# Performance work log

Measured on AMD Instinct MI355X. Metric: run time of the kernel, lower is better.

## Reference

```python
import math
import jax, jax.numpy as jnp
import numpy as np

HEADS = 8
DIM = 512
HEAD_SIZE = DIM // HEADS  # 64


def setup_inputs() -> dict:
    key = jax.random.key(0)
    ks = jax.random.split(key, 5)
    b, nh, nw, t, d = 16, 16, 16, 16, DIM
    x = jax.random.normal(ks[0], (b, nh, nw, t, d), dtype=jnp.float32)
    s = 1.0 / math.sqrt(d)
    Wq = jax.random.normal(ks[1], (d, d), dtype=jnp.float32) * s
    Wk = jax.random.normal(ks[2], (d, d), dtype=jnp.float32) * s
    Wv = jax.random.normal(ks[3], (d, d), dtype=jnp.float32) * s
    Wo = jax.random.normal(ks[4], (d, d), dtype=jnp.float32) * s
    z = jnp.zeros((d,), dtype=jnp.float32)
    return {"x": x, "Wq": Wq, "bq": z, "Wk": Wk, "bk": z, "Wv": Wv, "bv": z, "Wo": Wo, "bo": z}


def _split_heads(t):
    # [b, n1, n2, T, D] -> [b, n1, n2, H, T, hs]
    b, n1, n2, T, _ = t.shape
    return t.reshape(b, n1, n2, T, HEADS, HEAD_SIZE).transpose(0, 1, 2, 4, 3, 5)


def reference(x, Wq, bq, Wk, bk, Wv, bv, Wo, bo):
    q = _split_heads(x @ Wq + bq)
    k = _split_heads(x @ Wk + bk)
    v = _split_heads(x @ Wv + bv)
    # windowed attention scores: [b, n1, n2, H, T, T]
    scores = jnp.einsum('bnmhtd,bnmhsd->bnmhts', q, k) / math.sqrt(HEAD_SIZE)
    probs = jax.nn.sigmoid(scores)  # NOTE: elementwise sigmoid, not softmax
    ctx = jnp.einsum('bnmhts,bnmhsd->bnmhtd', probs, v)
    b, n1, n2, H, T, hs = ctx.shape
    ctx = ctx.transpose(0, 1, 2, 4, 3, 5).reshape(b, n1, n2, T, H * hs)
    return ctx @ Wo + bo
```

## Files before the change

### kernel.cpp

```cpp
#include <hip/hip_runtime.h>
#include <hip/hip_bf16.h>

typedef float f32x4 __attribute__((ext_vector_type(4)));
typedef __bf16 bf16x8 __attribute__((ext_vector_type(8)));
typedef unsigned short u16x4 __attribute__((ext_vector_type(4)));
typedef unsigned short u16x8 __attribute__((ext_vector_type(8)));

__device__ __forceinline__ unsigned short f2bf(float f) {
  union { float f; unsigned u; } x; x.f = f;
  unsigned r = x.u + 0x7FFFu + ((x.u >> 16) & 1u);
  return (unsigned short)(r >> 16);
}

__device__ __forceinline__ void gl16(const void* g, void* l) {
  __builtin_amdgcn_global_load_lds(
      (const __attribute__((address_space(1))) unsigned*)g,
      (__attribute__((address_space(3))) unsigned*)l, 16, 0, 0);
}

__global__ __launch_bounds__(256) void prep_wt(const float* __restrict__ Wq,
                                               const float* __restrict__ Wk,
                                               const float* __restrict__ Wv,
                                               const float* __restrict__ Wo,
                                               unsigned short* __restrict__ WT) {
  __shared__ unsigned short ts[64][65];
  const float* W = (blockIdx.z == 0) ? Wq : (blockIdx.z == 1) ? Wk
                   : (blockIdx.z == 2) ? Wv : Wo;
  const int t = threadIdx.x;
  const int kbase = blockIdx.y * 64;
  const int nbase = blockIdx.x * 64;
  for (int i = 0; i < 16; ++i) {
    int idx = i * 256 + t;
    int r = idx >> 6, c = idx & 63;
    ts[r][c] = f2bf(W[(size_t)(kbase + r) * 512 + nbase + c]);
  }
  __syncthreads();
  unsigned short* dst = WT + (size_t)blockIdx.z * 512 * 512;
  for (int i = 0; i < 16; ++i) {
    int idx = i * 256 + t;
    int nn = idx >> 6, kk = idx & 63;
    dst[(size_t)(nbase + nn) * 512 + kbase + kk] = ts[kk][nn];
  }
}

__global__ void prep_bias(const float* __restrict__ bq, const float* __restrict__ bk,
                          const float* __restrict__ bv, float* __restrict__ biasc) {
  int i = blockIdx.x * 256 + threadIdx.x;
  if (i < 512) biasc[i] = bq[i];
  else if (i < 1024) biasc[i] = bk[i - 512];
  else if (i < 1536) biasc[i] = bv[i - 1024];
}

__global__ __launch_bounds__(256) void convert_x(const float* __restrict__ x,
                                                 unsigned short* __restrict__ xb,
                                                 long long n8) {
  long long i = (long long)blockIdx.x * 256 + threadIdx.x;
  const long long stride = (long long)gridDim.x * 256;
  for (; i < n8; i += stride) {
    f32x4 a = *reinterpret_cast<const f32x4*>(&x[i * 8]);
    f32x4 b = *reinterpret_cast<const f32x4*>(&x[i * 8 + 4]);
    u16x8 o;
    o[0] = f2bf(a[0]); o[1] = f2bf(a[1]); o[2] = f2bf(a[2]); o[3] = f2bf(a[3]);
    o[4] = f2bf(b[0]); o[5] = f2bf(b[1]); o[6] = f2bf(b[2]); o[7] = f2bf(b[3]);
    *reinterpret_cast<u16x8*>(&xb[i * 8]) = o;
  }
}

template <typename CT>
__global__ __launch_bounds__(256, 4) void gemm128(
    const unsigned short* __restrict__ A, int lda,
    const unsigned short* __restrict__ BT,
    CT* __restrict__ C, int ldc,
    const float* __restrict__ bias, int NB) {
  __shared__ alignas(16) unsigned short pool[16640];
  const int t = threadIdx.x;
  const int lane = t & 63;
  const int w = t >> 6;
  const int wm = w >> 1, wn = w & 1;

  const int nwg = gridDim.x;
  const int cpx = nwg >> 3;
  const int wg = (blockIdx.x & 7) * cpx + (blockIdx.x >> 3);
  const int n0 = (wg % NB) * 128;
  const int m0 = (wg / NB) * 128;

  const int sgr = lane >> 2;
  const int sgc = ((lane & 3) ^ ((lane >> 3) & 3)) << 3;
  const unsigned short* gA = A + (size_t)(m0 + w * 32 + sgr) * lda + sgc;
  const unsigned short* gB = BT + (size_t)(n0 + w * 32 + sgr) * 512 + sgc;
  const int lw = w * 1024;

#define SA(kt, b)                                                           \
  { const unsigned short* g_ = gA + (kt) * 32;                              \
    gl16(g_, &pool[(b) * 4096 + lw]);                                       \
    gl16(g_ + (size_t)16 * lda, &pool[(b) * 4096 + lw + 512]); }
#define SB(kt, b)                                                           \
  { const unsigned short* g_ = gB + (kt) * 32;                              \
    gl16(g_, &pool[8192 + (b) * 4096 + lw]);                                \
    gl16(g_ + (size_t)16 * 512, &pool[8192 + (b) * 4096 + lw + 512]); }

  const int fr = lane & 15;
  const int fg = lane >> 4;
  const int aslot = (fg ^ ((fr >> 1) & 3)) << 3;

  f32x4 acc[4][4];
#pragma unroll
  for (int i = 0; i < 4; ++i)
#pragma unroll
    for (int j = 0; j < 4; ++j) acc[i][j] = (f32x4){0.f, 0.f, 0.f, 0.f};
  bf16x8 afr[4], bfr[4];

  SA(0, 0) SB(0, 0)
  asm volatile("s_waitcnt vmcnt(0)" ::: "memory");
  __builtin_amdgcn_s_barrier();

#pragma unroll
  for (int kt = 0; kt < 16; ++kt) {
    const int b = kt & 1;
    if (kt < 15) { SA(kt + 1, b ^ 1) SB(kt + 1, b ^ 1) }
#pragma unroll
    for (int mi = 0; mi < 4; ++mi)
      afr[mi] = *reinterpret_cast<const bf16x8*>(
          &pool[b * 4096 + (wm * 64 + mi * 16 + fr) * 32 + aslot]);
#pragma unroll
    for (int ni = 0; ni < 4; ++ni)
      bfr[ni] = *reinterpret_cast<const bf16x8*>(
          &pool[8192 + b * 4096 + (wn * 64 + ni * 16 + fr) * 32 + aslot]);
    asm volatile("s_waitcnt lgkmcnt(0)" ::: "memory");
    __builtin_amdgcn_sched_barrier(0);
    __builtin_amdgcn_s_setprio(1);
#pragma unroll
    for (int mi = 0; mi < 4; ++mi)
#pragma unroll
      for (int ni = 0; ni < 4; ++ni)
        acc[mi][ni] = __builtin_amdgcn_mfma_f32_16x16x32_bf16(
            afr[mi], bfr[ni], acc[mi][ni], 0, 0, 0);
    __builtin_amdgcn_s_setprio(0);
    asm volatile("s_waitcnt vmcnt(0)" ::: "memory");
    __builtin_amdgcn_s_barrier();
  }
#undef SA
#undef SB

  if constexpr (sizeof(CT) == 2) {
#pragma unroll
    for (int ni = 0; ni < 4; ++ni) {
      int cl = wn * 64 + ni * 16 + fr;
      float bc = bias[n0 + cl];
#pragma unroll
      for (int mi = 0; mi < 4; ++mi) {
        int rl = wm * 64 + mi * 16 + fg * 4;
#pragma unroll
        for (int r = 0; r < 4; ++r)
          pool[(rl + r) * 130 + cl] = f2bf(acc[mi][ni][r] + bc);
      }
    }
    __syncthreads();
#pragma unroll
    for (int it = 0; it < 8; ++it) {
      int idx = it * 256 + t;
      int row = idx >> 4, c8 = idx & 15;
      u16x8 v = *reinterpret_cast<const u16x8*>(&pool[row * 130 + c8 * 8]);
      *reinterpret_cast<u16x8*>(&C[(size_t)(m0 + row) * ldc + n0 + c8 * 8]) = v;
    }
  } else {
    float* stf = reinterpret_cast<float*>(pool);
#pragma unroll
    for (int h = 0; h < 2; ++h) {
      if (wm == h) {
#pragma unroll
        for (int ni = 0; ni < 4; ++ni) {
          int cl = wn * 64 + ni * 16 + fr;
          float bc = bias[n0 + cl];
#pragma unroll
          for (int mi = 0; mi < 4; ++mi) {
            int rl = mi * 16 + fg * 4;
#pragma unroll
            for (int r = 0; r < 4; ++r)
              stf[(rl + r) * 130 + cl] = acc[mi][ni][r] + bc;
          }
        }
      }
      __syncthreads();
#pragma unroll
      for (int it = 0; it < 8; ++it) {
        int idx = it * 256 + t;
        int row = idx >> 5, c4 = idx & 31;
        f32x4 v = *reinterpret_cast<const f32x4*>(&stf[row * 130 + c4 * 4]);
        *reinterpret_cast<f32x4*>(
            &C[(size_t)(m0 + h * 64 + row) * ldc + n0 + c4 * 4]) = v;
      }
      __syncthreads();
    }
  }
}

__global__ __launch_bounds__(256) void attn2(unsigned short* __restrict__ QKV) {
  __shared__ alignas(16) unsigned short sh[33792];
  const int VS = 16384, PS = 32768;
  const int t = threadIdx.x;
  const int lane = t & 63;
  const int w = t >> 6;
  const int fr = lane & 15, fg = lane >> 4, fx = lane & 7;
  const int sr = lane >> 3;
  const int sgx = ((lane & 7) ^ sr) << 3;
  const int sgl = (lane & 7) << 3;
  const size_t m0r = (size_t)blockIdx.x * 128;

#define SK2(h, b)                                                            \
  _Pragma("unroll") for (int u = 0; u < 4; ++u) {                            \
    const int r0 = u * 32 + w * 8;                                           \
    gl16(QKV + (m0r + r0 + sr) * 1536 + 512 + (h) * 64 + sgx,                \
         &sh[(b) * 8192 + r0 * 64]);                                         \
  }
#define SV2(h, b)                                                            \
  _Pragma("unroll") for (int u = 0; u < 4; ++u) {                            \
    const int r0 = u * 32 + w * 8;                                           \
    gl16(QKV + (m0r + r0 + sr) * 1536 + 1024 + (h) * 64 + sgl,               \
         &sh[VS + (b) * 8192 + r0 * 64]);                                    \
  }

  SK2(0, 0) SV2(0, 0)
  asm volatile("s_waitcnt vmcnt(0)" ::: "memory");
  __syncthreads();

  for (int h = 0; h < 8; ++h) {
    const int b = h & 1;
    u16x8 q[2][2];
#pragma unroll
    for (int ww = 0; ww < 2; ++ww) {
      const int wi = w * 2 + ww;
      const unsigned short* qrow = QKV + (m0r + wi * 16 + fr) * 1536 + h * 64;
      q[ww][0] = *reinterpret_cast<const u16x8*>(qrow + fg * 8);
      q[ww][1] = *reinterpret_cast<const u16x8*>(qrow + 32 + fg * 8);
    }
    if (h < 7) { SK2(h + 1, b ^ 1) SV2(h + 1, b ^ 1) }

#pragma unroll
    for (int ww = 0; ww < 2; ++ww) {
      const int wi = w * 2 + ww;
      f32x4 s = (f32x4){0.f, 0.f, 0.f, 0.f};
      {
        bf16x8 kf_ = *reinterpret_cast<const bf16x8*>(
            &sh[b * 8192 + (wi * 16 + fr) * 64 + ((fg ^ fx) << 3)]);
        s = __builtin_amdgcn_mfma_f32_16x16x32_bf16(
            kf_, __builtin_bit_cast(bf16x8, q[ww][0]), s, 0, 0, 0);
        kf_ = *reinterpret_cast<const bf16x8*>(
            &sh[b * 8192 + (wi * 16 + fr) * 64 + (((4 + fg) ^ fx) << 3)]);
        s = __builtin_amdgcn_mfma_f32_16x16x32_bf16(
            kf_, __builtin_bit_cast(bf16x8, q[ww][1]), s, 0, 0, 0);
      }
      u16x4 pfu;
#pragma unroll
      for (int r = 0; r < 4; ++r)
        pfu[r] = f2bf(1.0f / (1.0f + __expf(-s[r] * 0.125f)));
      *reinterpret_cast<u16x4*>(&sh[PS + w * 256 + fr * 16 + fg * 4]) = pfu;
      u16x8 pbu = (u16x8){0, 0, 0, 0, 0, 0, 0, 0};
      if (fg < 2)
        pbu = *reinterpret_cast<const u16x8*>(&sh[PS + w * 256 + fr * 16 + fg * 8]);
      bf16x8 pb = __builtin_bit_cast(bf16x8, pbu);
#pragma unroll
      for (int dc = 0; dc < 4; ++dc) {
        u16x8 vau;
#pragma unroll
        for (int j = 0; j < 8; ++j)
          vau[j] = sh[VS + b * 8192 + (wi * 16 + (fg & 1) * 8 + j) * 64 + dc * 16 + fr];
        f32x4 c = __builtin_amdgcn_mfma_f32_16x16x32_bf16(
            __builtin_bit_cast(bf16x8, vau), pb, (f32x4){0.f, 0.f, 0.f, 0.f},
            0, 0, 0);
        u16x4 o;
#pragma unroll
        for (int r = 0; r < 4; ++r) o[r] = f2bf(c[r]);
        *reinterpret_cast<u16x4*>(
            &QKV[(m0r + wi * 16 + fr) * 1536 + 1024 + h * 64 + dc * 16 + fg * 4]) = o;
      }
    }
    asm volatile("s_waitcnt vmcnt(8)" ::: "memory");
    __syncthreads();
  }
#undef SK2
#undef SV2
}

extern "C" void kernel_launch(void* const* d_in, const int* in_sizes, int n_in,
                              void* d_out, int out_size, void* d_ws, size_t ws_size,
                              hipStream_t stream) {
  const float* x  = (const float*)d_in[0];
  const float* Wq = (const float*)d_in[1];
  const float* bq = (const float*)d_in[2];
  const float* Wk = (const float*)d_in[3];
  const float* bk = (const float*)d_in[4];
  const float* Wv = (const float*)d_in[5];
  const float* bv = (const float*)d_in[6];
  const float* Wo = (const float*)d_in[7];
  const float* bo = (const float*)d_in[8];
  float* out = (float*)d_out;

  const int M = 65536;
  char* ws = (char*)d_ws;
  unsigned short* WT = (unsigned short*)ws;
  float* biasc = (float*)(ws + (size_t)2048 * 512 * 2);
  const long long prep_bytes = (long long)2048 * 512 * 2 + 8192;

  prep_wt<<<dim3(8, 8, 4), 256, 0, stream>>>(Wq, Wk, Wv, Wo, WT);
  prep_bias<<<6, 256, 0, stream>>>(bq, bk, bv, biasc);

  long long avail = (long long)ws_size - prep_bytes;
  int chunk_rows = 65536;
  while (chunk_rows > 2048 && (long long)chunk_rows * 4096 > avail) chunk_rows >>= 1;
  const int nchunks = M / chunk_rows;

  unsigned short* Xb  = (unsigned short*)(ws + prep_bytes);
  unsigned short* QKV = Xb + (size_t)chunk_rows * 512;

  for (int c = 0; c < nchunks; ++c) {
    const size_t row0 = (size_t)c * chunk_rows;
    const int mt = chunk_rows / 128;
    convert_x<<<2048, 256, 0, stream>>>(x + row0 * 512, Xb,
                                        (long long)chunk_rows * 64);
    gemm128<unsigned short><<<mt * 12, 256, 0, stream>>>(
        Xb, 512, WT, QKV, 1536, biasc, 12);
    attn2<<<chunk_rows / 128, 256, 0, stream>>>(QKV);
    gemm128<float><<<mt * 4, 256, 0, stream>>>(
        QKV + 1024, 1536, WT + (size_t)1536 * 512, out + row0 * 512, 512, bo, 4);
  }
}
```

Measured before the change: 294.2 us.

## Fuse fp32-to-bf16 conversion of x into the QKV GEMM A-tile loads

```diff
diff --git a/kernel.cpp b/kernel.cpp
--- a/kernel.cpp
+++ b/kernel.cpp
@@ -51,18 +51,114 @@
   else if (i < 1536) biasc[i] = bv[i - 1024];
 }
 
-__global__ __launch_bounds__(256) void convert_x(const float* __restrict__ x,
-                                                 unsigned short* __restrict__ xb,
-                                                 long long n8) {
-  long long i = (long long)blockIdx.x * 256 + threadIdx.x;
-  const long long stride = (long long)gridDim.x * 256;
-  for (; i < n8; i += stride) {
-    f32x4 a = *reinterpret_cast<const f32x4*>(&x[i * 8]);
-    f32x4 b = *reinterpret_cast<const f32x4*>(&x[i * 8 + 4]);
-    u16x8 o;
-    o[0] = f2bf(a[0]); o[1] = f2bf(a[1]); o[2] = f2bf(a[2]); o[3] = f2bf(a[3]);
-    o[4] = f2bf(b[0]); o[5] = f2bf(b[1]); o[6] = f2bf(b[2]); o[7] = f2bf(b[3]);
-    *reinterpret_cast<u16x8*>(&xb[i * 8]) = o;
+__global__ __launch_bounds__(256, 3) void gemm128_f32(
+    const float* __restrict__ A, int lda,
+    const unsigned short* __restrict__ BT,
+    unsigned short* __restrict__ C, int ldc,
+    const float* __restrict__ bias, int NB) {
+  __shared__ alignas(16) unsigned short pool[24576];
+  const int t = threadIdx.x;
+  const int lane = t & 63;
+  const int w = t >> 6;
+  const int wm = w >> 1, wn = w & 1;
+
+  const int nwg = gridDim.x;
+  const int cpx = nwg >> 3;
+  const int wg = (blockIdx.x & 7) * cpx + (blockIdx.x >> 3);
+  const int n0 = (wg % NB) * 128;
+  const int m0 = (wg / NB) * 128;
+
+  const int sgr8 = lane >> 3;
+  const int sga = ((lane & 7) ^ sgr8) << 2;
+  const float* gAf = A + (size_t)(m0 + w * 32 + sgr8) * lda + sga;
+  const int sgr = lane >> 2;
+  const int sgc = ((lane & 3) ^ ((lane >> 3) & 3)) << 3;
+  const unsigned short* gB = BT + (size_t)(n0 + w * 32 + sgr) * 512 + sgc;
+
+#define SAF(kt, b)                                                          \
+  _Pragma("unroll") for (int u = 0; u < 4; ++u) {                           \
+    gl16(gAf + (size_t)(u) * 8 * lda + (kt) * 32,                           \
+         &pool[(b) * 8192 + (w * 32 + u * 8) * 64]);                        \
+  }
+#define SB(kt, b)                                                           \
+  { const unsigned short* g_ = gB + (kt) * 32;                              \
+    gl16(g_, &pool[16384 + (b) * 4096 + w * 1024]);                         \
+    gl16(g_ + (size_t)16 * 512, &pool[16384 + (b) * 4096 + w * 1024 + 512]); }
+
+  const int fr = lane & 15;
+  const int fg = lane >> 4;
+  const int bslot = (fg ^ ((fr >> 1) & 3)) << 3;
+  const float* apf = reinterpret_cast<const float*>(pool);
+
+  f32x4 acc[4][4];
+#pragma unroll
+  for (int i = 0; i < 4; ++i)
+#pragma unroll
+    for (int j = 0; j < 4; ++j) acc[i][j] = (f32x4){0.f, 0.f, 0.f, 0.f};
+  bf16x8 afr[4], bfr[4];
+
+  SAF(0, 0) SB(0, 0)
+  asm volatile("s_waitcnt vmcnt(0)" ::: "memory");
+  __builtin_amdgcn_s_barrier();
+
+#pragma unroll
+  for (int kt = 0; kt < 16; ++kt) {
+    const int b = kt & 1;
+    if (kt < 15) { SAF(kt + 1, b ^ 1) SB(kt + 1, b ^ 1) }
+#pragma unroll
+    for (int mi = 0; mi < 4; ++mi) {
+      const int r = wm * 64 + mi * 16 + fr;
+      const int s0 = ((2 * fg) ^ (fr & 7)) << 2;
+      const int s1 = ((2 * fg + 1) ^ (fr & 7)) << 2;
+      f32x4 lo = *reinterpret_cast<const f32x4*>(&apf[b * 4096 + r * 32 + s0]);
+      f32x4 hi = *reinterpret_cast<const f32x4*>(&apf[b * 4096 + r * 32 + s1]);
+      bf16x8 o;
+#pragma unroll
+      for (int j = 0; j < 4; ++j) {
+        o[j] = (__bf16)lo[j];
+        o[4 + j] = (__bf16)hi[j];
+      }
+      afr[mi] = o;
+    }
+#pragma unroll
+    for (int ni = 0; ni < 4; ++ni)
+      bfr[ni] = *reinterpret_cast<const bf16x8*>(
+          &pool[16384 + b * 4096 + (wn * 64 + ni * 16 + fr) * 32 + bslot]);
+    asm volatile("s_waitcnt lgkmcnt(0)" ::: "memory");
+    __builtin_amdgcn_sched_barrier(0);
+    __builtin_amdgcn_s_setprio(1);
+#pragma unroll
+    for (int mi = 0; mi < 4; ++mi)
+#pragma unroll
+      for (int ni = 0; ni < 4; ++ni)
+        acc[mi][ni] = __builtin_amdgcn_mfma_f32_16x16x32_bf16(
+            afr[mi], bfr[ni], acc[mi][ni], 0, 0, 0);
+    __builtin_amdgcn_s_setprio(0);
+    asm volatile("s_waitcnt vmcnt(0)" ::: "memory");
+    __builtin_amdgcn_s_barrier();
+  }
+#undef SAF
+#undef SB
+
+#pragma unroll
+  for (int ni = 0; ni < 4; ++ni) {
+    int cl = wn * 64 + ni * 16 + fr;
+    float bc = bias[n0 + cl];
+#pragma unroll
+    for (int mi = 0; mi < 4; ++mi) {
+      int rl = wm * 64 + mi * 16 + fg * 4;
+#pragma unroll
+      for (int r = 0; r < 4; ++r)
+        pool[(rl + r) * 130 + cl] = f2bf(acc[mi][ni][r] + bc);
+    }
+  }
+  __syncthreads();
+#pragma unroll
+  for (int it = 0; it < 8; ++it) {
+    int idx = it * 256 + t;
+    int row = idx >> 4, c8 = idx & 15;
+    u16x8 v = *reinterpret_cast<const u16x8*>(&pool[row * 130 + c8 * 8]);
+    *reinterpret_cast<u16x8*>(&C[(size_t)(m0 + row) * ldc + n0 + c8 * 8]) = v;
   }
 }
 
@@ -307,19 +403,16 @@
 
   long long avail = (long long)ws_size - prep_bytes;
   int chunk_rows = 65536;
-  while (chunk_rows > 2048 && (long long)chunk_rows * 4096 > avail) chunk_rows >>= 1;
+  while (chunk_rows > 2048 && (long long)chunk_rows * 3072 > avail) chunk_rows >>= 1;
   const int nchunks = M / chunk_rows;
 
-  unsigned short* Xb  = (unsigned short*)(ws + prep_bytes);
-  unsigned short* QKV = Xb + (size_t)chunk_rows * 512;
+  unsigned short* QKV = (unsigned short*)(ws + prep_bytes);
 
   for (int c = 0; c < nchunks; ++c) {
     const size_t row0 = (size_t)c * chunk_rows;
     const int mt = chunk_rows / 128;
-    convert_x<<<2048, 256, 0, stream>>>(x + row0 * 512, Xb,
-                                        (long long)chunk_rows * 64);
-    gemm128<unsigned short><<<mt * 12, 256, 0, stream>>>(
-        Xb, 512, WT, QKV, 1536, biasc, 12);
+    gemm128_f32<<<mt * 12, 256, 0, stream>>>(
+        x + row0 * 512, 512, WT, QKV, 1536, biasc, 12);
     attn2<<<chunk_rows / 128, 256, 0, stream>>>(QKV);
     gemm128<float><<<mt * 4, 256, 0, stream>>>(
         QKV + 1024, 1536, WT + (size_t)1536 * 512, out + row0 * 512, 512, bo, 4);
```

Result: slower. 315.7 us (+7.3%).
